# Optimization experiments

Measured on AMD Instinct MI355X. Metric: run time of the kernel, lower is better.

The kernel has to match this reference:

```python
import jax, jax.numpy as jnp
import numpy as np

D_MODEL = 1024
N_HEADS = 16
D_K = D_MODEL // N_HEADS


def setup_inputs() -> dict:
    key = jax.random.key(0)
    ks = jax.random.split(key, 10)
    s = 1.0 / np.sqrt(D_MODEL)
    def lin(k):
        kw, kb = jax.random.split(k)
        W = jax.random.uniform(kw, (D_MODEL, D_MODEL), jnp.float32, -s, s)
        b = jax.random.uniform(kb, (D_MODEL,), jnp.float32, -s, s)
        return W, b
    Wq, bq = lin(ks[0])
    Wk, bk = lin(ks[1])
    Wv, bv = lin(ks[2])
    Wo, bo = lin(ks[3])
    x = jax.random.normal(ks[4], (2, 2048, D_MODEL), jnp.float32)
    gamma = jnp.ones((D_MODEL,), jnp.float32)
    beta = jnp.zeros((D_MODEL,), jnp.float32)
    return {"x": x, "Wq": Wq, "bq": bq, "Wk": Wk, "bk": bk,
            "Wv": Wv, "bv": bv, "Wo": Wo, "bo": bo,
            "gamma": gamma, "beta": beta}


def _mha(x, Wq, bq, Wk, bk, Wv, bv, Wo, bo, gamma, beta):
    B, S, _ = x.shape
    residual = x
    # Linear uses y = x @ W.T + b (torch nn.Linear convention)
    q = (x @ Wq.T + bq).reshape(B, S, N_HEADS, D_K).transpose(0, 2, 1, 3)
    k = (x @ Wk.T + bk).reshape(B, S, N_HEADS, D_K).transpose(0, 2, 1, 3)
    v = (x @ Wv.T + bv).reshape(B, S, N_HEADS, D_K).transpose(0, 2, 1, 3)
    scores = jnp.einsum("bhqd,bhkd->bhqk", q, k) / jnp.sqrt(jnp.float32(D_K))
    attn = jax.nn.softmax(scores, axis=-1)
    out = jnp.einsum("bhqk,bhkd->bhqd", attn, v)
    out = out.transpose(0, 2, 1, 3).reshape(B, S, D_MODEL)
    out = out @ Wo.T + bo
    h = out + residual
    mu = jnp.mean(h, axis=-1, keepdims=True)
    var = jnp.var(h, axis=-1, keepdims=True)
    h = (h - mu) / jnp.sqrt(var + 1e-5) * gamma + beta
    return jnp.where(h >= 0, h, 0.01 * h)


def reference(x, Wq, bq, Wk, bk, Wv, bv, Wo, bo, gamma, beta):
    return _mha(x, Wq, bq, Wk, bk, Wv, bv, Wo, bo, gamma, beta)
```

## Files before the change

### kernel.cpp

```cpp
#include <hip/hip_runtime.h>

#define DM   1024
#define NH   16
#define DK   64
#define SEQ  2048
#define BATCH 2

typedef __attribute__((ext_vector_type(8))) short bf16x8;
typedef __attribute__((ext_vector_type(4))) float f32x4;

__device__ __forceinline__ unsigned short f2bf(float f) {
    unsigned int u = __builtin_bit_cast(unsigned int, f);
    u += 0x7FFFu + ((u >> 16) & 1u);
    return (unsigned short)(u >> 16);
}

__global__ __launch_bounds__(256)
void cvt_kernel(const float* __restrict__ x,
                const float* __restrict__ wq, const float* __restrict__ wk,
                const float* __restrict__ wv, const float* __restrict__ wo,
                unsigned short* __restrict__ xb,
                unsigned short* __restrict__ wqkvb,
                unsigned short* __restrict__ wob)
{
    const int seg = blockIdx.y;
    const float* src;
    unsigned short* dst;
    int n;
    if (seg == 0)      { src = x;  dst = xb;                  n = 4 << 20; }
    else if (seg == 1) { src = wq; dst = wqkvb;               n = 1 << 20; }
    else if (seg == 2) { src = wk; dst = wqkvb + (1 << 20);   n = 1 << 20; }
    else if (seg == 3) { src = wv; dst = wqkvb + (2 << 20);   n = 1 << 20; }
    else               { src = wo; dst = wob;                 n = 1 << 20; }
    for (int i = (blockIdx.x * 256 + threadIdx.x) * 4; i < n; i += 1024 * 256 * 4) {
        const float4 v = *reinterpret_cast<const float4*>(&src[i]);
        ushort4 o;
        o.x = f2bf(v.x); o.y = f2bf(v.y); o.z = f2bf(v.z); o.w = f2bf(v.w);
        *reinterpret_cast<ushort4*>(&dst[i]) = o;
    }
}

template <int MODE, int BN>
__global__ __launch_bounds__(256)
void gemm2_kernel(const unsigned short* __restrict__ Ab,
                  const unsigned short* __restrict__ Wall,
                  const float* __restrict__ B0, const float* __restrict__ B1,
                  const float* __restrict__ B2,
                  unsigned short* __restrict__ q_ws,
                  unsigned short* __restrict__ k_ws,
                  unsigned short* __restrict__ vt_ws,
                  const float* __restrict__ resid,
                  float* __restrict__ h_ws)
{
    __shared__ unsigned short sA[128 * 32];
    __shared__ unsigned short sB[BN * 32];

    const int tid = threadIdx.x, lane = tid & 63, wid = tid >> 6;
    const int n0 = blockIdx.x * BN, m0 = blockIdx.y * 128;
    const int z  = (MODE == 0) ? blockIdx.z : 0;
    const unsigned short* W = Wall + (size_t)z * (1 << 20);
    const float* bias = (MODE == 0) ? (z == 0 ? B0 : (z == 1 ? B1 : B2)) : B0;

    const int g = lane >> 4, lq = lane & 15;
    const int wr = wid >> 1, wc = wid & 1;
    const int rA = lane >> 2;
    const int csh = (lane & 3) * 8;

    f32x4 acc[4][BN / 32] = {};

    for (int k0 = 0; k0 < DM; k0 += 32) {
        #pragma unroll
        for (int i = 0; i < 2; ++i) {
            const int c = wid * 2 + i;
            __builtin_amdgcn_global_load_lds(
                (const __attribute__((address_space(1))) unsigned int*)
                    &Ab[(size_t)(m0 + c * 16 + rA) * DM + k0 + csh],
                (__attribute__((address_space(3))) unsigned int*)&sA[c * 512],
                16, 0, 0);
        }
        #pragma unroll
        for (int i = 0; i < BN / 64; ++i) {
            const int c = wid * (BN / 64) + i;
            __builtin_amdgcn_global_load_lds(
                (const __attribute__((address_space(1))) unsigned int*)
                    &W[(size_t)(n0 + c * 16 + rA) * DM + k0 + csh],
                (__attribute__((address_space(3))) unsigned int*)&sB[c * 512],
                16, 0, 0);
        }
        __syncthreads();

        bf16x8 a[4], b[BN / 32];
        #pragma unroll
        for (int m = 0; m < 4; ++m)
            a[m] = *reinterpret_cast<const bf16x8*>(&sA[(wr * 64 + m * 16 + lq) * 32 + 8 * g]);
        #pragma unroll
        for (int n = 0; n < BN / 32; ++n)
            b[n] = *reinterpret_cast<const bf16x8*>(&sB[(wc * (BN / 2) + n * 16 + lq) * 32 + 8 * g]);
        #pragma unroll
        for (int m = 0; m < 4; ++m)
            #pragma unroll
            for (int n = 0; n < BN / 32; ++n)
                acc[m][n] = __builtin_amdgcn_mfma_f32_16x16x32_bf16(
                    a[m], b[n], acc[m][n], 0, 0, 0);
        __syncthreads();
    }

    #pragma unroll
    for (int m = 0; m < 4; ++m) {
        #pragma unroll
        for (int n = 0; n < BN / 32; ++n) {
            #pragma unroll
            for (int j = 0; j < 4; ++j) {
                const int row = m0 + wr * 64 + m * 16 + 4 * g + j;
                const int col = n0 + wc * (BN / 2) + n * 16 + lq;
                float v = acc[m][n][j] + bias[col];
                if constexpr (MODE == 0) {
                    const int b_ = row >> 11, s = row & (SEQ - 1);
                    const int hh = col >> 6,  d = col & (DK - 1);
                    if (z == 0)
                        q_ws[(((size_t)(b_ * NH + hh) * SEQ + s) << 6) + d] = f2bf(v * 0.18033688f);
                    else if (z == 1)
                        k_ws[(((size_t)(b_ * NH + hh) * SEQ + s) << 6) + d] = f2bf(v);
                    else
                        vt_ws[((size_t)(b_ * NH + hh) * DK + d) * SEQ + s] = f2bf(v);
                } else {
                    const size_t idx = (size_t)row * DM + col;
                    h_ws[idx] = v + resid[idx];
                }
            }
        }
    }
}

__global__ __launch_bounds__(256)
void attn_kernel(const unsigned short* __restrict__ q_ws,
                 const unsigned short* __restrict__ k_ws,
                 const unsigned short* __restrict__ vt_ws,
                 unsigned short* __restrict__ ao_ws)
{
    __shared__ unsigned short lds4[4][4096];

    const int tid = threadIdx.x;
    const int lane = tid & 63, wid = tid >> 6;
    const int g = lane >> 4, lq = lane & 15;
    const int bh = blockIdx.y;
    const int q0 = blockIdx.x * 64;

    const size_t qbase = ((size_t)bh * SEQ + q0 + wid * 16 + lq) * DK;
    const bf16x8 aq0 = *reinterpret_cast<const bf16x8*>(&q_ws[qbase + 8 * g]);
    const bf16x8 aq1 = *reinterpret_cast<const bf16x8*>(&q_ws[qbase + 32 + 8 * g]);

    const short one_bf = (short)0x3F80;
    const bf16x8 onesf = {one_bf, one_bf, one_bf, one_bf, one_bf, one_bf, one_bf, one_bf};

    const int l8 = lane >> 3, l7 = lane & 7;
    const int scol = 8 * (l7 ^ l8);
    const int r7 = lq & 7;
    const int ck0 = 8 * (g ^ r7);
    const int ck1 = 8 * ((4 + g) ^ r7);

    const unsigned short* kp0 = &k_ws [((size_t)bh * SEQ + wid * 16 + l8) * DK + scol];
    const unsigned short* kp1 = kp0 + 8 * DK;
    const unsigned short* vp0 = &vt_ws[((size_t)bh * DK  + wid * 16 + l8) * SEQ + scol];
    const unsigned short* vp1 = vp0 + 8 * SEQ;

    const unsigned short* pK0 = &lds4[0][lq * 64 + ck0];
    const unsigned short* pK1 = &lds4[0][lq * 64 + ck1];
    const unsigned short* pV0 = &lds4[2][lq * 64 + ck0];
    const unsigned short* pV1 = &lds4[2][lq * 64 + ck1];

    f32x4 oacc[4] = {};
    f32x4 lacc = {};

    const int dst0 = wid * 2 * 512, dst1 = (wid * 2 + 1) * 512;

    auto stage = [&](int kbuf) {
        __builtin_amdgcn_global_load_lds(
            (const __attribute__((address_space(1))) unsigned int*)kp0,
            (__attribute__((address_space(3))) unsigned int*)&lds4[kbuf][dst0], 16, 0, 0);
        __builtin_amdgcn_global_load_lds(
            (const __attribute__((address_space(1))) unsigned int*)kp1,
            (__attribute__((address_space(3))) unsigned int*)&lds4[kbuf][dst1], 16, 0, 0);
        __builtin_amdgcn_global_load_lds(
            (const __attribute__((address_space(1))) unsigned int*)vp0,
            (__attribute__((address_space(3))) unsigned int*)&lds4[2 + kbuf][dst0], 16, 0, 0);
        __builtin_amdgcn_global_load_lds(
            (const __attribute__((address_space(1))) unsigned int*)vp1,
            (__attribute__((address_space(3))) unsigned int*)&lds4[2 + kbuf][dst1], 16, 0, 0);
        kp0 += 64 * DK; kp1 += 64 * DK;
        vp0 += 64;      vp1 += 64;
    };

    auto compute = [&](int OFF) {
        f32x4 st[4];
        __builtin_amdgcn_s_setprio(1);
        #pragma unroll
        for (int kb = 0; kb < 4; ++kb) {
            const bf16x8 k0 = *reinterpret_cast<const bf16x8*>(pK0 + OFF + kb * 1024);
            const bf16x8 k1 = *reinterpret_cast<const bf16x8*>(pK1 + OFF + kb * 1024);
            f32x4 zz = {};
            zz = __builtin_amdgcn_mfma_f32_16x16x32_bf16(k0, aq0, zz, 0, 0, 0);
            zz = __builtin_amdgcn_mfma_f32_16x16x32_bf16(k1, aq1, zz, 0, 0, 0);
            st[kb] = zz;
        }
        __builtin_amdgcn_s_setprio(0);

        unsigned int pk[4][2];
        #pragma unroll
        for (int kb = 0; kb < 4; ++kb) {
            float e0 = exp2f(st[kb][0]);
            float e1 = exp2f(st[kb][1]);
            float e2 = exp2f(st[kb][2]);
            float e3 = exp2f(st[kb][3]);
            asm("v_cvt_pk_bf16_f32 %0, %1, %2" : "=v"(pk[kb][0]) : "v"(e0), "v"(e1));
            asm("v_cvt_pk_bf16_f32 %0, %1, %2" : "=v"(pk[kb][1]) : "v"(e2), "v"(e3));
        }

        const int s01 = ((2 * g) & 3) * 16 + lq;
        const int s23 = ((2 * g + 1) & 3) * 16 + lq;
        const bool hi = (g >= 2);
        bf16x8 pf[2];
        #pragma unroll
        for (int m = 0; m < 2; ++m) {
            const unsigned int w0A = __shfl(pk[2 * m][0], s01), w0B = __shfl(pk[2 * m + 1][0], s01);
            const unsigned int w1A = __shfl(pk[2 * m][1], s01), w1B = __shfl(pk[2 * m + 1][1], s01);
            const unsigned int w2A = __shfl(pk[2 * m][0], s23), w2B = __shfl(pk[2 * m + 1][0], s23);
            const unsigned int w3A = __shfl(pk[2 * m][1], s23), w3B = __shfl(pk[2 * m + 1][1], s23);
            uint4 ww;
            ww.x = hi ? w0B : w0A;
            ww.y = hi ? w1B : w1A;
            ww.z = hi ? w2B : w2A;
            ww.w = hi ? w3B : w3A;
            pf[m] = __builtin_bit_cast(bf16x8, ww);
        }

        __builtin_amdgcn_s_setprio(1);
        lacc = __builtin_amdgcn_mfma_f32_16x16x32_bf16(onesf, pf[0], lacc, 0, 0, 0);
        lacc = __builtin_amdgcn_mfma_f32_16x16x32_bf16(onesf, pf[1], lacc, 0, 0, 0);
        #pragma unroll
        for (int db = 0; db < 4; ++db) {
            const bf16x8 v0 = *reinterpret_cast<const bf16x8*>(pV0 + OFF + db * 1024);
            const bf16x8 v1 = *reinterpret_cast<const bf16x8*>(pV1 + OFF + db * 1024);
            oacc[db] = __builtin_amdgcn_mfma_f32_16x16x32_bf16(v0, pf[0], oacc[db], 0, 0, 0);
            oacc[db] = __builtin_amdgcn_mfma_f32_16x16x32_bf16(v1, pf[1], oacc[db], 0, 0, 0);
        }
        __builtin_amdgcn_s_setprio(0);
    };

    stage(0);
    __syncthreads();

    for (int tt = 0; tt < 16; ++tt) {
        stage(1);
        compute(0);
        __syncthreads();
        if (tt < 15) stage(0);
        compute(4096);
        __syncthreads();
    }

    const int b_ = bh >> 4, hh = bh & 15;
    const int qg = q0 + wid * 16 + lq;
    const float rl = 1.0f / lacc[0];
    #pragma unroll
    for (int db = 0; db < 4; ++db) {
        ushort4 o;
        o.x = f2bf(oacc[db][0] * rl);
        o.y = f2bf(oacc[db][1] * rl);
        o.z = f2bf(oacc[db][2] * rl);
        o.w = f2bf(oacc[db][3] * rl);
        *reinterpret_cast<ushort4*>(
            &ao_ws[(size_t)(b_ * SEQ + qg) * DM + hh * 64 + db * 16 + 4 * g]) = o;
    }
}

__global__ __launch_bounds__(256)
void ln_kernel(const float* __restrict__ h, const float* __restrict__ gamma,
               const float* __restrict__ beta, float* __restrict__ out)
{
    __shared__ float s1[4], s2[4];
    const int row = blockIdx.x, tid = threadIdx.x;
    const float4 v = reinterpret_cast<const float4*>(h + (size_t)row * DM)[tid];
    float sum = v.x + v.y + v.z + v.w;
    float sq  = v.x * v.x + v.y * v.y + v.z * v.z + v.w * v.w;
    #pragma unroll
    for (int mk = 1; mk <= 32; mk <<= 1) {
        sum += __shfl_xor(sum, mk);
        sq  += __shfl_xor(sq, mk);
    }
    if ((tid & 63) == 0) { s1[tid >> 6] = sum; s2[tid >> 6] = sq; }
    __syncthreads();
    sum = s1[0] + s1[1] + s1[2] + s1[3];
    sq  = s2[0] + s2[1] + s2[2] + s2[3];
    const float mu = sum * (1.f / DM);
    const float var = sq * (1.f / DM) - mu * mu;
    const float rstd = rsqrtf(var + 1e-5f);
    const float4 gv = reinterpret_cast<const float4*>(gamma)[tid];
    const float4 bv = reinterpret_cast<const float4*>(beta)[tid];
    float4 o;
    o.x = (v.x - mu) * rstd * gv.x + bv.x;
    o.y = (v.y - mu) * rstd * gv.y + bv.y;
    o.z = (v.z - mu) * rstd * gv.z + bv.z;
    o.w = (v.w - mu) * rstd * gv.w + bv.w;
    o.x = o.x >= 0.f ? o.x : 0.01f * o.x;
    o.y = o.y >= 0.f ? o.y : 0.01f * o.y;
    o.z = o.z >= 0.f ? o.z : 0.01f * o.z;
    o.w = o.w >= 0.f ? o.w : 0.01f * o.w;
    reinterpret_cast<float4*>(out + (size_t)row * DM)[tid] = o;
}

extern "C" void kernel_launch(void* const* d_in, const int* in_sizes, int n_in,
                              void* d_out, int out_size, void* d_ws, size_t ws_size,
                              hipStream_t stream)
{
    const float* x     = (const float*)d_in[0];
    const float* Wq    = (const float*)d_in[1];
    const float* bq    = (const float*)d_in[2];
    const float* Wk    = (const float*)d_in[3];
    const float* bk    = (const float*)d_in[4];
    const float* Wv    = (const float*)d_in[5];
    const float* bv    = (const float*)d_in[6];
    const float* Wo    = (const float*)d_in[7];
    const float* bo    = (const float*)d_in[8];
    const float* gamma = (const float*)d_in[9];
    const float* beta  = (const float*)d_in[10];

    char* ws = (char*)d_ws;
    unsigned short* q_ws   = (unsigned short*)(ws);
    unsigned short* k_ws   = (unsigned short*)(ws + (8u << 20));
    unsigned short* vt_ws  = (unsigned short*)(ws + (16u << 20));
    unsigned short* ao_ws  = (unsigned short*)(ws + (24u << 20));
    unsigned short* xb_ws  = (unsigned short*)(ws + (32u << 20));
    unsigned short* wqkv_b = (unsigned short*)(ws + (40u << 20));
    unsigned short* wo_b   = (unsigned short*)(ws + (46u << 20));
    float* h_ws = (float*)ws;

    const dim3 blk(256);
    cvt_kernel<<<dim3(1024, 5), blk, 0, stream>>>(
        x, Wq, Wk, Wv, Wo, xb_ws, wqkv_b, wo_b);
    gemm2_kernel<0, 128><<<dim3(8, 32, 3), blk, 0, stream>>>(
        xb_ws, wqkv_b, bq, bk, bv, q_ws, k_ws, vt_ws, nullptr, nullptr);
    attn_kernel<<<dim3(32, 32), blk, 0, stream>>>(q_ws, k_ws, vt_ws, ao_ws);
    gemm2_kernel<1, 64><<<dim3(16, 32, 1), blk, 0, stream>>>(
        ao_ws, wo_b, bo, nullptr, nullptr, nullptr, nullptr, nullptr, x, h_ws);
    ln_kernel<<<dim3(4096), blk, 0, stream>>>(h_ws, gamma, beta, (float*)d_out);
}
```

Measured before the change: 152.0 us.

## Switch attention to 32x32 MFMA tiles with 128-query blocks and permlane32 swaps

The attention kernel now has each wave handle 32 query rows using 32x32x16 bf16 MFMAs instead of 16x16x32, and each block covers 128 queries, so the grid halves. The P-matrix relayout uses v_permlane32_swap in place of multiple __shfl calls. LDS staging is doubled to four K/V buffers, so two 64-key tiles are loaded per barrier, halving the number of syncs. The aim is fewer shuffles, more K/V reuse per LDS load and denser matrix instructions. The cost is higher register and LDS pressure and only 512 blocks, which lowers occupancy.

```diff
diff --git a/kernel.cpp b/kernel.cpp
--- a/kernel.cpp
+++ b/kernel.cpp
@@ -8,6 +8,7 @@
 
 typedef __attribute__((ext_vector_type(8))) short bf16x8;
 typedef __attribute__((ext_vector_type(4))) float f32x4;
+typedef __attribute__((ext_vector_type(16))) float f32x16;
 
 __device__ __forceinline__ unsigned short f2bf(float f) {
     unsigned int u = __builtin_bit_cast(unsigned int, f);
@@ -138,39 +139,43 @@
                  const unsigned short* __restrict__ vt_ws,
                  unsigned short* __restrict__ ao_ws)
 {
-    __shared__ unsigned short lds4[4][4096];
+    __shared__ unsigned short lds4[8][4096];
 
     const int tid = threadIdx.x;
     const int lane = tid & 63, wid = tid >> 6;
-    const int g = lane >> 4, lq = lane & 15;
+    const int l31 = lane & 31, h = lane >> 5;
     const int bh = blockIdx.y;
-    const int q0 = blockIdx.x * 64;
-
-    const size_t qbase = ((size_t)bh * SEQ + q0 + wid * 16 + lq) * DK;
-    const bf16x8 aq0 = *reinterpret_cast<const bf16x8*>(&q_ws[qbase + 8 * g]);
-    const bf16x8 aq1 = *reinterpret_cast<const bf16x8*>(&q_ws[qbase + 32 + 8 * g]);
+    const int q0 = blockIdx.x * 128;
+    const int q  = q0 + wid * 32 + l31;
+
+    const size_t qbase = ((size_t)bh * SEQ + q) * DK;
+    bf16x8 qf[4];
+    #pragma unroll
+    for (int j = 0; j < 4; ++j)
+        qf[j] = *reinterpret_cast<const bf16x8*>(&q_ws[qbase + j * 16 + h * 8]);
 
     const short one_bf = (short)0x3F80;
     const bf16x8 onesf = {one_bf, one_bf, one_bf, one_bf, one_bf, one_bf, one_bf, one_bf};
 
     const int l8 = lane >> 3, l7 = lane & 7;
     const int scol = 8 * (l7 ^ l8);
-    const int r7 = lq & 7;
-    const int ck0 = 8 * (g ^ r7);
-    const int ck1 = 8 * ((4 + g) ^ r7);
-
     const unsigned short* kp0 = &k_ws [((size_t)bh * SEQ + wid * 16 + l8) * DK + scol];
     const unsigned short* kp1 = kp0 + 8 * DK;
     const unsigned short* vp0 = &vt_ws[((size_t)bh * DK  + wid * 16 + l8) * SEQ + scol];
     const unsigned short* vp1 = vp0 + 8 * SEQ;
 
-    const unsigned short* pK0 = &lds4[0][lq * 64 + ck0];
-    const unsigned short* pK1 = &lds4[0][lq * 64 + ck1];
-    const unsigned short* pV0 = &lds4[2][lq * 64 + ck0];
-    const unsigned short* pV1 = &lds4[2][lq * 64 + ck1];
-
-    f32x4 oacc[4] = {};
-    f32x4 lacc = {};
+    const int r7 = l31 & 7;
+    const unsigned short* pK[4];
+    const unsigned short* pV[4];
+    #pragma unroll
+    for (int j = 0; j < 4; ++j) {
+        const int ck = 8 * (((j << 1) + h) ^ r7);
+        pK[j] = &lds4[0][l31 * 64 + ck];
+        pV[j] = &lds4[4][l31 * 64 + ck];
+    }
+
+    f32x16 oacc[2] = {};
+    f32x16 lacc = {};
 
     const int dst0 = wid * 2 * 512, dst1 = (wid * 2 + 1) * 512;
 
@@ -183,94 +188,104 @@
             (__attribute__((address_space(3))) unsigned int*)&lds4[kbuf][dst1], 16, 0, 0);
         __builtin_amdgcn_global_load_lds(
             (const __attribute__((address_space(1))) unsigned int*)vp0,
-            (__attribute__((address_space(3))) unsigned int*)&lds4[2 + kbuf][dst0], 16, 0, 0);
+            (__attribute__((address_space(3))) unsigned int*)&lds4[4 + kbuf][dst0], 16, 0, 0);
         __builtin_amdgcn_global_load_lds(
             (const __attribute__((address_space(1))) unsigned int*)vp1,
-            (__attribute__((address_space(3))) unsigned int*)&lds4[2 + kbuf][dst1], 16, 0, 0);
+            (__attribute__((address_space(3))) unsigned int*)&lds4[4 + kbuf][dst1], 16, 0, 0);
         kp0 += 64 * DK; kp1 += 64 * DK;
         vp0 += 64;      vp1 += 64;
     };
 
     auto compute = [&](int OFF) {
-        f32x4 st[4];
+        f32x16 st0 = {}, st1 = {};
         __builtin_amdgcn_s_setprio(1);
         #pragma unroll
-        for (int kb = 0; kb < 4; ++kb) {
-            const bf16x8 k0 = *reinterpret_cast<const bf16x8*>(pK0 + OFF + kb * 1024);
-            const bf16x8 k1 = *reinterpret_cast<const bf16x8*>(pK1 + OFF + kb * 1024);
-            f32x4 zz = {};
-            zz = __builtin_amdgcn_mfma_f32_16x16x32_bf16(k0, aq0, zz, 0, 0, 0);
-            zz = __builtin_amdgcn_mfma_f32_16x16x32_bf16(k1, aq1, zz, 0, 0, 0);
-            st[kb] = zz;
+        for (int j = 0; j < 4; ++j) {
+            const bf16x8 k0 = *reinterpret_cast<const bf16x8*>(pK[j] + OFF);
+            const bf16x8 k1 = *reinterpret_cast<const bf16x8*>(pK[j] + OFF + 2048);
+            st0 = __builtin_amdgcn_mfma_f32_32x32x16_bf16(k0, qf[j], st0, 0, 0, 0);
+            st1 = __builtin_amdgcn_mfma_f32_32x32x16_bf16(k1, qf[j], st1, 0, 0, 0);
         }
         __builtin_amdgcn_s_setprio(0);
 
-        unsigned int pk[4][2];
-        #pragma unroll
-        for (int kb = 0; kb < 4; ++kb) {
-            float e0 = exp2f(st[kb][0]);
-            float e1 = exp2f(st[kb][1]);
-            float e2 = exp2f(st[kb][2]);
-            float e3 = exp2f(st[kb][3]);
-            asm("v_cvt_pk_bf16_f32 %0, %1, %2" : "=v"(pk[kb][0]) : "v"(e0), "v"(e1));
-            asm("v_cvt_pk_bf16_f32 %0, %1, %2" : "=v"(pk[kb][1]) : "v"(e2), "v"(e3));
-        }
-
-        const int s01 = ((2 * g) & 3) * 16 + lq;
-        const int s23 = ((2 * g + 1) & 3) * 16 + lq;
-        const bool hi = (g >= 2);
-        bf16x8 pf[2];
-        #pragma unroll
-        for (int m = 0; m < 2; ++m) {
-            const unsigned int w0A = __shfl(pk[2 * m][0], s01), w0B = __shfl(pk[2 * m + 1][0], s01);
-            const unsigned int w1A = __shfl(pk[2 * m][1], s01), w1B = __shfl(pk[2 * m + 1][1], s01);
-            const unsigned int w2A = __shfl(pk[2 * m][0], s23), w2B = __shfl(pk[2 * m + 1][0], s23);
-            const unsigned int w3A = __shfl(pk[2 * m][1], s23), w3B = __shfl(pk[2 * m + 1][1], s23);
-            uint4 ww;
-            ww.x = hi ? w0B : w0A;
-            ww.y = hi ? w1B : w1A;
-            ww.z = hi ? w2B : w2A;
-            ww.w = hi ? w3B : w3A;
-            pf[m] = __builtin_bit_cast(bf16x8, ww);
+        bf16x8 pb[4];
+        #pragma unroll
+        for (int s = 0; s < 2; ++s) {
+            #pragma unroll
+            for (int jg = 0; jg < 2; ++jg) {
+                const int rb = 8 * jg;
+                float e0, e1, e2, e3, e4, e5, e6, e7;
+                if (s == 0) {
+                    e0 = exp2f(st0[rb + 0]); e1 = exp2f(st0[rb + 1]);
+                    e2 = exp2f(st0[rb + 2]); e3 = exp2f(st0[rb + 3]);
+                    e4 = exp2f(st0[rb + 4]); e5 = exp2f(st0[rb + 5]);
+                    e6 = exp2f(st0[rb + 6]); e7 = exp2f(st0[rb + 7]);
+                } else {
+                    e0 = exp2f(st1[rb + 0]); e1 = exp2f(st1[rb + 1]);
+                    e2 = exp2f(st1[rb + 2]); e3 = exp2f(st1[rb + 3]);
+                    e4 = exp2f(st1[rb + 4]); e5 = exp2f(st1[rb + 5]);
+                    e6 = exp2f(st1[rb + 6]); e7 = exp2f(st1[rb + 7]);
+                }
+                unsigned int wA, wB, wC, wD;
+                asm("v_cvt_pk_bf16_f32 %0, %1, %2" : "=v"(wA) : "v"(e0), "v"(e1));
+                asm("v_cvt_pk_bf16_f32 %0, %1, %2" : "=v"(wB) : "v"(e2), "v"(e3));
+                asm("v_cvt_pk_bf16_f32 %0, %1, %2" : "=v"(wC) : "v"(e4), "v"(e5));
+                asm("v_cvt_pk_bf16_f32 %0, %1, %2" : "=v"(wD) : "v"(e6), "v"(e7));
+                asm("v_permlane32_swap_b32 %0, %1" : "+v"(wA), "+v"(wC));
+                asm("v_permlane32_swap_b32 %0, %1" : "+v"(wB), "+v"(wD));
+                uint4 ww;
+                ww.x = wA; ww.y = wB; ww.z = wC; ww.w = wD;
+                pb[2 * s + jg] = __builtin_bit_cast(bf16x8, ww);
+            }
         }
 
         __builtin_amdgcn_s_setprio(1);
-        lacc = __builtin_amdgcn_mfma_f32_16x16x32_bf16(onesf, pf[0], lacc, 0, 0, 0);
-        lacc = __builtin_amdgcn_mfma_f32_16x16x32_bf16(onesf, pf[1], lacc, 0, 0, 0);
-        #pragma unroll
-        for (int db = 0; db < 4; ++db) {
-            const bf16x8 v0 = *reinterpret_cast<const bf16x8*>(pV0 + OFF + db * 1024);
-            const bf16x8 v1 = *reinterpret_cast<const bf16x8*>(pV1 + OFF + db * 1024);
-            oacc[db] = __builtin_amdgcn_mfma_f32_16x16x32_bf16(v0, pf[0], oacc[db], 0, 0, 0);
-            oacc[db] = __builtin_amdgcn_mfma_f32_16x16x32_bf16(v1, pf[1], oacc[db], 0, 0, 0);
-        }
+        #pragma unroll
+        for (int jg = 0; jg < 4; ++jg)
+            lacc = __builtin_amdgcn_mfma_f32_32x32x16_bf16(onesf, pb[jg], lacc, 0, 0, 0);
+        #pragma unroll
+        for (int dt = 0; dt < 2; ++dt)
+            #pragma unroll
+            for (int jg = 0; jg < 4; ++jg) {
+                const bf16x8 vv = *reinterpret_cast<const bf16x8*>(pV[jg] + OFF + dt * 2048);
+                oacc[dt] = __builtin_amdgcn_mfma_f32_32x32x16_bf16(vv, pb[jg], oacc[dt], 0, 0, 0);
+            }
         __builtin_amdgcn_s_setprio(0);
     };
 
     stage(0);
+    stage(1);
     __syncthreads();
 
-    for (int tt = 0; tt < 16; ++tt) {
-        stage(1);
-        compute(0);
+    #pragma unroll 1
+    for (int tt = 0; tt < 7; ++tt) {
+        stage(2); stage(3);
+        compute(0); compute(4096);
         __syncthreads();
-        if (tt < 15) stage(0);
-        compute(4096);
+        stage(0); stage(1);
+        compute(8192); compute(12288);
         __syncthreads();
     }
 
+    stage(2); stage(3);
+    compute(0); compute(4096);
+    __syncthreads();
+    compute(8192); compute(12288);
+
     const int b_ = bh >> 4, hh = bh & 15;
-    const int qg = q0 + wid * 16 + lq;
     const float rl = 1.0f / lacc[0];
-    #pragma unroll
-    for (int db = 0; db < 4; ++db) {
-        ushort4 o;
-        o.x = f2bf(oacc[db][0] * rl);
-        o.y = f2bf(oacc[db][1] * rl);
-        o.z = f2bf(oacc[db][2] * rl);
-        o.w = f2bf(oacc[db][3] * rl);
-        *reinterpret_cast<ushort4*>(
-            &ao_ws[(size_t)(b_ * SEQ + qg) * DM + hh * 64 + db * 16 + 4 * g]) = o;
+    unsigned short* aop = &ao_ws[(size_t)(b_ * SEQ + q) * DM + hh * 64];
+    #pragma unroll
+    for (int dt = 0; dt < 2; ++dt) {
+        #pragma unroll
+        for (int qd = 0; qd < 4; ++qd) {
+            ushort4 o;
+            o.x = f2bf(oacc[dt][4 * qd + 0] * rl);
+            o.y = f2bf(oacc[dt][4 * qd + 1] * rl);
+            o.z = f2bf(oacc[dt][4 * qd + 2] * rl);
+            o.w = f2bf(oacc[dt][4 * qd + 3] * rl);
+            *reinterpret_cast<ushort4*>(&aop[dt * 32 + 8 * qd + 4 * h]) = o;
+        }
     }
 }
 
@@ -340,7 +355,7 @@
         x, Wq, Wk, Wv, Wo, xb_ws, wqkv_b, wo_b);
     gemm2_kernel<0, 128><<<dim3(8, 32, 3), blk, 0, stream>>>(
         xb_ws, wqkv_b, bq, bk, bv, q_ws, k_ws, vt_ws, nullptr, nullptr);
-    attn_kernel<<<dim3(32, 32), blk, 0, stream>>>(q_ws, k_ws, vt_ws, ao_ws);
+    attn_kernel<<<dim3(16, 32), blk, 0, stream>>>(q_ws, k_ws, vt_ws, ao_ws);
     gemm2_kernel<1, 64><<<dim3(16, 32, 1), blk, 0, stream>>>(
         ao_ws, wo_b, bo, nullptr, nullptr, nullptr, nullptr, nullptr, x, h_ws);
     ln_kernel<<<dim3(4096), blk, 0, stream>>>(h_ws, gamma, beta, (float*)d_out);
```

After: 137.5 us. 1.11x faster.
